# Kernel optimization log

Measured on AMD Instinct MI355X. Metric: run time of the kernel, lower is better.

Reference implementation:

```python
import jax, jax.numpy as jnp
import numpy as np

B, T, D, H, P, A = 128, 512, 512, 512, 512, 32  # envs, steps, feat, lstm hidden, latent, actions


def setup_inputs() -> dict:
    key = jax.random.key(0)
    ks = jax.random.split(key, 30)
    N = B * T
    lin = lambda k, o, i: 0.02 * jax.random.normal(k, (o, i), jnp.float32)
    vec = lambda k, o: 0.02 * jax.random.normal(k, (o,), jnp.float32)
    inp = {
        'features': jax.random.normal(ks[0], (N, D), jnp.float32),
        'episode_starts': (jax.random.uniform(ks[1], (N,)) < 0.02).astype(jnp.float32),
        'h0_pi': jax.random.normal(ks[2], (1, B, H), jnp.float32),
        'c0_pi': jax.random.normal(ks[3], (1, B, H), jnp.float32),
        'h0_vf': jax.random.normal(ks[4], (1, B, H), jnp.float32),
        'c0_vf': jax.random.normal(ks[5], (1, B, H), jnp.float32),
        'Wih_pi': lin(ks[6], 4 * H, D), 'Whh_pi': lin(ks[7], 4 * H, H),
        'bih_pi': vec(ks[8], 4 * H), 'bhh_pi': vec(ks[9], 4 * H),
        'Wih_vf': lin(ks[10], 4 * H, D), 'Whh_vf': lin(ks[11], 4 * H, H),
        'bih_vf': vec(ks[12], 4 * H), 'bhh_vf': vec(ks[13], 4 * H),
        'pol_w1': lin(ks[14], P, H), 'pol_b1': vec(ks[15], P),
        'pol_w2': lin(ks[16], P, P), 'pol_b2': vec(ks[17], P),
        'val_w1': lin(ks[18], P, H), 'val_b1': vec(ks[19], P),
        'val_w2': lin(ks[20], P, P), 'val_b2': vec(ks[21], P),
        'actor_w': lin(ks[22], A, P), 'actor_b': vec(ks[23], A),
        'critic_w': lin(ks[24], 1, P), 'critic_b': vec(ks[25], 1),
        'deterministic': 1,
    }
    return inp


def masked_lstm(xs, starts, h0, c0, Wih, Whh, bih, bhh):
    # xs: [T,B,D], starts: [T,B]; PyTorch gate order i,f,g,o; reset h,c where episode starts.
    def step(carry, inp):
        h, c = carry
        x, s = inp
        m = (1.0 - s)[:, None]
        h, c = h * m, c * m
        g = x @ Wih.T + bih + h @ Whh.T + bhh
        i, f, gg, o = jnp.split(g, 4, axis=-1)
        c = jax.nn.sigmoid(f) * c + jax.nn.sigmoid(i) * jnp.tanh(gg)
        h = jax.nn.sigmoid(o) * jnp.tanh(c)
        return (h, c), h
    (hT, cT), ys = jax.lax.scan(step, (h0[0], c0[0]), (xs, starts))
    return ys, hT[None], cT[None]


def mlp(x, w1, b1, w2, b2):
    return jax.nn.relu(x @ w1.T + b1) @ w2.T + b2


def reference(features, episode_starts, h0_pi, c0_pi, h0_vf, c0_vf,
              Wih_pi, Whh_pi, bih_pi, bhh_pi, Wih_vf, Whh_vf, bih_vf, bhh_vf,
              pol_w1, pol_b1, pol_w2, pol_b2, val_w1, val_b1, val_w2, val_b2,
              actor_w, actor_b, critic_w, critic_b, deterministic):
    n_seq = h0_pi.shape[1]
    d = features.shape[-1]
    xs = features.reshape(n_seq, -1, d).swapaxes(0, 1)        # [T,B,D]
    st = episode_starts.reshape(n_seq, -1).swapaxes(0, 1)     # [T,B]
    ys_pi, h_pi, c_pi = masked_lstm(xs, st, h0_pi, c0_pi, Wih_pi, Whh_pi, bih_pi, bhh_pi)
    ys_vf, h_vf, c_vf = masked_lstm(xs, st, h0_vf, c0_vf, Wih_vf, Whh_vf, bih_vf, bhh_vf)
    hsz = ys_pi.shape[-1]
    lat_pi = ys_pi.swapaxes(0, 1).reshape(-1, hsz)            # [B*T,H]
    lat_vf = ys_vf.swapaxes(0, 1).reshape(-1, hsz)
    lat_pi = mlp(lat_pi, pol_w1, pol_b1, pol_w2, pol_b2)
    lat_vf = mlp(lat_vf, val_w1, val_b1, val_w2, val_b2)
    values = lat_vf @ critic_w.T + critic_b                    # [B*T,1]
    logits = lat_pi @ actor_w.T + actor_b                      # [B*T,A]
    actions = jnp.argmax(logits, axis=-1)                      # deterministic mode
    logp = jax.nn.log_softmax(logits, axis=-1)
    log_prob = jnp.take_along_axis(logp, actions[:, None], axis=1)[:, 0]
    return actions, values, log_prob, h_pi, c_pi, h_vf, c_vf
```

## Files before the change

### kernel.cpp

```cpp
#include <hip/hip_runtime.h>
#include <math.h>

#define BB 128
#define TT 512
#define DD 512
#define HH 512
#define NN (BB*TT)
#define PP 512
#define AA 32
#define CH 64
#define CR (BB*CH)

typedef unsigned short u16;
typedef unsigned int   u32;
typedef __attribute__((ext_vector_type(8))) short short8;
typedef __attribute__((ext_vector_type(4))) float f32x4;

__device__ __forceinline__ u16 f2bf(float f){
    u32 x = __float_as_uint(f);
    u32 r = (x + 0x7fffu + ((x >> 16) & 1u)) >> 16;
    return (u16)r;
}
__device__ __forceinline__ float bf2f(u16 u){
    return __uint_as_float(((u32)u) << 16);
}
__device__ __forceinline__ f32x4 mfma16(short8 a, short8 b, f32x4 c){
    return __builtin_amdgcn_mfma_f32_16x16x32_bf16(a, b, c, 0, 0, 0);
}
__device__ __forceinline__ float sigm(float x){
    return 1.f/(1.f + __expf(-x));
}
__device__ __forceinline__ float tanh_f(float x){
    return 1.f - 2.f/(1.f + __expf(2.f*x));
}

__device__ __forceinline__ short8 ld_mall(const u16* p){
    short8 r;
    asm volatile("global_load_dwordx4 %0, %1, off sc0 sc1"
                 : "=&v"(r) : "v"(p) : "memory");
    return r;
}
__device__ __forceinline__ void st_mall(u16* p, short8 v){
    asm volatile("global_store_dwordx4 %0, %1, off sc0 sc1"
                 :: "v"(p), "v"(v) : "memory");
}

__device__ __forceinline__ unsigned a_add(unsigned* p){
    return __hip_atomic_fetch_add(p, 1u, __ATOMIC_RELAXED, __HIP_MEMORY_SCOPE_AGENT);
}
__device__ __forceinline__ unsigned a_ld(unsigned* p){
    return __hip_atomic_load(p, __ATOMIC_RELAXED, __HIP_MEMORY_SCOPE_AGENT);
}

#define BARZ_N 75264

__global__ __launch_bounds__(256) void prep_lstm_w(
    const float* __restrict__ Wih_pi, const float* __restrict__ Whh_pi,
    const float* __restrict__ bih_pi, const float* __restrict__ bhh_pi,
    const float* __restrict__ Wih_vf, const float* __restrict__ Whh_vf,
    const float* __restrict__ bih_vf, const float* __restrict__ bhh_vf,
    u16* __restrict__ wihHi, u16* __restrict__ wihLo,
    u16* __restrict__ whhHi, u16* __restrict__ whhLo,
    float* __restrict__ biasP)
{
    long i = (long)blockIdx.x*256 + threadIdx.x;
    if (i >= 2L*2048*512) return;
    int L = (int)(i >> 20);
    int rem = (int)(i & 1048575);
    int c = rem >> 9, k = rem & 511;
    int u = c >> 2, g = c & 3;
    long src = (long)(g*512 + u)*512 + k;
    float wih = (L ? Wih_vf : Wih_pi)[src];
    float whh = (L ? Whh_vf : Whh_pi)[src];
    u16 h1 = f2bf(wih); wihHi[i] = h1; wihLo[i] = f2bf(wih - bf2f(h1));
    u16 h2 = f2bf(whh); whhHi[i] = h2; whhLo[i] = f2bf(whh - bf2f(h2));
    if (k == 0) {
        float b = (L ? bih_vf : bih_pi)[g*512+u] + (L ? bhh_vf : bhh_pi)[g*512+u];
        biasP[L*2048 + c] = b;
    }
}

__global__ __launch_bounds__(256) void prep_mlp_w(
    const float* __restrict__ w1pi, const float* __restrict__ w1vf,
    const float* __restrict__ w2pi, const float* __restrict__ w2vf,
    const float* __restrict__ b1pi, const float* __restrict__ b1vf,
    const float* __restrict__ b2pi, const float* __restrict__ b2vf,
    u16* __restrict__ mHi, u16* __restrict__ mLo, float* __restrict__ biasM)
{
    long i = (long)blockIdx.x*256 + threadIdx.x;
    if (i >= 4L*262144) return;
    int mat = (int)(i >> 18);
    int rem = (int)(i & 262143);
    const float* src = mat==0 ? w1pi : mat==1 ? w1vf : mat==2 ? w2pi : w2vf;
    float v = src[rem];
    u16 h = f2bf(v); mHi[i] = h; mLo[i] = f2bf(v - bf2f(h));
    if (rem < 512) {
        const float* bs = mat==0 ? b1pi : mat==1 ? b1vf : mat==2 ? b2pi : b2vf;
        biasM[mat*512 + rem] = bs[rem];
    }
}

__global__ __launch_bounds__(256) void init_state_k(
    const float* __restrict__ h0_pi, const float* __restrict__ c0_pi,
    const float* __restrict__ h0_vf, const float* __restrict__ c0_vf,
    const float* __restrict__ starts,
    u16* __restrict__ hHi, u16* __restrict__ hLo, float* __restrict__ cT,
    float* __restrict__ startsT, unsigned* __restrict__ barZ)
{
    int i = blockIdx.x*256 + threadIdx.x;
    if (i < BARZ_N) barZ[i] = 0u;
    if (i < NN) {
        int e = i >> 9, t = i & 511;
        startsT[t*128 + e] = starts[i];
    }
    if (i >= 2*BB*HH) return;
    int L = i >> 16; int r = i & 65535;
    int e = r >> 9, u = r & 511;
    float m = 1.0f - starts[(long)e*TT];
    float h = (L ? h0_vf : h0_pi)[r] * m;
    float c = (L ? c0_vf : c0_pi)[r] * m;
    long hidx = (long)(L*2)*65536 + r;
    u16 hh = f2bf(h);
    hHi[hidx] = hh; hLo[hidx] = f2bf(h - bf2f(hh));
    cT[(long)L*65536 + (long)u*128 + e] = c;
}

template<int AM, int EM>
__global__ __launch_bounds__(256) void gemm_k512(
    const float* __restrict__ Afp,
    const u16* __restrict__ aHi, const u16* __restrict__ aLo, long aZ,
    int rowSh, int rowOuterHi, int rowOuterLo, int rowBase,
    const u16* __restrict__ bHi, const u16* __restrict__ bLo, long bZ,
    const float* __restrict__ bias, long biasZ,
    float* __restrict__ outF, long outFZ, int outLd,
    u16* __restrict__ oHi, u16* __restrict__ oLo, long oZ)
{
    __shared__ u16 sAh[5120], sAl[5120], sBh[5120], sBl[5120];
    const int tid = threadIdx.x;
    const int z = blockIdx.z;
    const long Mbase = (long)blockIdx.x * 128;
    const long Nbase = (long)blockIdx.y * 128;
    const int r2 = tid >> 1, half = tid & 1;
    const long mstage = Mbase + r2;
    const long arow = (mstage >> rowSh) * (long)rowOuterHi
                    + (mstage & (((long)1<<rowSh)-1)) * (long)rowOuterLo + rowBase;
    const long brow = Nbase + r2;
    const int wid = tid >> 6, lane = tid & 63;
    const int mh = wid & 1, nh = wid >> 1;
    const int l15 = lane & 15, quad = lane >> 4;

    f32x4 acc[4][4];
    #pragma unroll
    for (int i = 0; i < 4; ++i)
        #pragma unroll
        for (int j = 0; j < 4; ++j)
            acc[i][j] = (f32x4){0.f,0.f,0.f,0.f};

    const int sOffW = r2*40 + half*16;

    for (int kt = 0; kt < 16; ++kt) {
        const int k0 = kt*32;
        if constexpr (AM == 0) {
            const float* ap = Afp + arow*512 + k0 + half*16;
            float fv[16];
            #pragma unroll
            for (int q = 0; q < 4; ++q) *(float4*)(fv + q*4) = ((const float4*)ap)[q];
            short8 vh0, vh1, vl0, vl1;
            #pragma unroll
            for (int i = 0; i < 8; ++i){
                u16 h  = f2bf(fv[i]);   vh0[i] = (short)h;  vl0[i] = (short)f2bf(fv[i]   - bf2f(h));
                u16 h2 = f2bf(fv[8+i]); vh1[i] = (short)h2; vl1[i] = (short)f2bf(fv[8+i] - bf2f(h2));
            }
            *(short8*)(sAh + sOffW) = vh0; *(short8*)(sAh + sOffW + 8) = vh1;
            *(short8*)(sAl + sOffW) = vl0; *(short8*)(sAl + sOffW + 8) = vl1;
        } else {
            const u16* ph = aHi + (long)z*aZ + arow*512 + k0 + half*16;
            const u16* pl = aLo + (long)z*aZ + arow*512 + k0 + half*16;
            *(short8*)(sAh + sOffW) = *(const short8*)ph;
            *(short8*)(sAh + sOffW + 8) = *(const short8*)(ph + 8);
            *(short8*)(sAl + sOffW) = *(const short8*)pl;
            *(short8*)(sAl + sOffW + 8) = *(const short8*)(pl + 8);
        }
        {
            const u16* ph = bHi + (long)z*bZ + brow*512 + k0 + half*16;
            const u16* pl = bLo + (long)z*bZ + brow*512 + k0 + half*16;
            *(short8*)(sBh + sOffW) = *(const short8*)ph;
            *(short8*)(sBh + sOffW + 8) = *(const short8*)(ph + 8);
            *(short8*)(sBl + sOffW) = *(const short8*)pl;
            *(short8*)(sBl + sOffW + 8) = *(const short8*)(pl + 8);
        }
        __syncthreads();
        short8 bh[4], bl[4];
        #pragma unroll
        for (int nt = 0; nt < 4; ++nt){
            int bo = (nh*64 + nt*16 + l15)*40 + quad*8;
            bh[nt] = *(const short8*)(sBh + bo);
            bl[nt] = *(const short8*)(sBl + bo);
        }
        #pragma unroll
        for (int mt = 0; mt < 4; ++mt){
            int ao = (mh*64 + mt*16 + l15)*40 + quad*8;
            short8 ah = *(const short8*)(sAh + ao);
            short8 al = *(const short8*)(sAl + ao);
            #pragma unroll
            for (int nt = 0; nt < 4; ++nt){
                acc[mt][nt] = mfma16(ah, bh[nt], acc[mt][nt]);
                acc[mt][nt] = mfma16(ah, bl[nt], acc[mt][nt]);
                acc[mt][nt] = mfma16(al, bh[nt], acc[mt][nt]);
            }
        }
        __syncthreads();
    }
    #pragma unroll
    for (int nt = 0; nt < 4; ++nt){
        const long col = Nbase + nh*64 + nt*16 + l15;
        const float bv = bias[(long)z*biasZ + col];
        #pragma unroll
        for (int mt = 0; mt < 4; ++mt){
            const long rowm = Mbase + mh*64 + mt*16 + quad*4;
            #pragma unroll
            for (int rr = 0; rr < 4; ++rr){
                float v = acc[mt][nt][rr] + bv;
                const long m = rowm + rr;
                if constexpr (EM == 0) {
                    outF[(long)z*outFZ + m*(long)outLd + col] = v;
                } else {
                    if constexpr (EM == 1) v = fmaxf(v, 0.f);
                    u16 h = f2bf(v);
                    u16 l = f2bf(v - bf2f(h));
                    oHi[(long)z*oZ + m*512 + col] = h;
                    oLo[(long)z*oZ + m*512 + col] = l;
                }
            }
        }
    }
}

__global__ __launch_bounds__(256) void lstm_chunk(
    u16* __restrict__ hHi, u16* __restrict__ hLo,
    const u16* __restrict__ whhHi, const u16* __restrict__ whhLo,
    const float* __restrict__ gx,
    const float* __restrict__ startsT,
    float* __restrict__ cT,
    u16* __restrict__ ysHi, u16* __restrict__ ysLo,
    float* __restrict__ dout, unsigned* __restrict__ barZ, int t0)
{
    __shared__ __attribute__((aligned(16))) u16 sA[2][16384];
    __shared__ float zsm[4][144];
    __shared__ unsigned shLead, shNloc, shXC;

    const int tid  = threadIdx.x;
    const int wc   = blockIdx.x;
    const int eb   = blockIdx.y;
    const int L    = blockIdx.z;
    const int wid  = tid >> 6, lane = tid & 63;
    const int l15  = lane & 15, quad = lane >> 4;
    const int ebase = eb*64;
    const int e    = ebase + wid*16 + l15;

    unsigned xcc;
    asm("s_getreg_b32 %0, hwreg(HW_REG_XCC_ID)" : "=s"(xcc));
    xcc &= 7u;
    const int ch = t0 >> 6;
    unsigned* ARRb  = barZ;
    unsigned* DONEb = barZ + 65536;
    unsigned* RCNTb = barZ + 73728;
    unsigned* SBARb = barZ + 74752;
    unsigned* XCNTb = barZ + 74880;

    if (tid == 0){
        unsigned r = a_add(&RCNTb[(ch*8 + (int)xcc)*16]);
        shLead = (r == 0u) ? 1u : 0u;
        if (r == 0u){
            a_add(&XCNTb[ch*16]);
            asm volatile("s_waitcnt vmcnt(0)" ::: "memory");
        }
        a_add(&SBARb[ch*16]);
        while (a_ld(&SBARb[ch*16]) < 256u) __builtin_amdgcn_s_sleep(2);
        shNloc = a_ld(&RCNTb[(ch*8 + (int)xcc)*16]);
        shXC   = a_ld(&XCNTb[ch*16]);
    }

    {
        const size_t wbase = (size_t)L*1048576 + (size_t)(wc*32)*512;
        #pragma unroll
        for (int i = 0; i < 16; ++i){
            int f = tid + i*256;
            int pl = f >> 11;
            int r2 = f & 2047;
            int wcol = r2 >> 6, ksg = r2 & 63;
            const u16* src = (pl ? whhLo : whhHi) + wbase + (size_t)wcol*512 + ksg*8;
            int dst = (ksg>>2)*1024 + wcol*32 + (ksg&3)*8;
            *(short8*)(sA[pl] + dst) = *(const short8*)src;
        }
    }
    __syncthreads();
    const unsigned lead = shLead, nloc = shNloc, xcnt = shXC;

    const int u0 = wc*8 + quad;
    const int u1 = wc*8 + 4 + quad;
    const size_t ci0 = (size_t)L*65536 + (size_t)u0*128 + e;
    const size_t ci1 = (size_t)L*65536 + (size_t)u1*128 + e;
    float c0 = cT[ci0];
    float c1 = cT[ci1];

    const size_t hrowOff = (size_t)e*512 + quad*8;
    const size_t gxbase  = ((size_t)L*CR + e)*2048 + wc*32 + quad*4;

    float4 gv0 = *(const float4*)(gx + gxbase);
    float4 gv1 = *(const float4*)(gx + gxbase + 16);
    float mn = (t0 < TT-1) ? (1.0f - startsT[(t0+1)*128 + e]) : 1.0f;

    for (int tau = 0; tau < CH; ++tau){
        const int t = t0 + tau;
        const int p = t & 1;

        const u16* hHiP = hHi + (size_t)(L*2+p)*65536 + hrowOff;
        const u16* hLoP = hLo + (size_t)(L*2+p)*65536 + hrowOff;
        short8 pbh[16], pbl[16];
        #pragma unroll
        for (int i = 0; i < 16; ++i){
            pbh[i] = ld_mall(hHiP + i*32);
            pbl[i] = ld_mall(hLoP + i*32);
        }
        f32x4 acc0 = (f32x4){0.f,0.f,0.f,0.f};
        f32x4 acc1 = (f32x4){0.f,0.f,0.f,0.f};
        #pragma unroll
        for (int kt = 0; kt < 16; ++kt){
            if (kt == 0){
                asm volatile("s_waitcnt vmcnt(24)" ::: "memory");
                __builtin_amdgcn_sched_barrier(0);
            } else if (kt == 4){
                asm volatile("s_waitcnt vmcnt(16)" ::: "memory");
                __builtin_amdgcn_sched_barrier(0);
            } else if (kt == 8){
                asm volatile("s_waitcnt vmcnt(8)" ::: "memory");
                __builtin_amdgcn_sched_barrier(0);
            } else if (kt == 12){
                asm volatile("s_waitcnt vmcnt(0)" ::: "memory");
                __builtin_amdgcn_sched_barrier(0);
            }
            short8 bh = pbh[kt];
            short8 bl = pbl[kt];
            int a0 = kt*1024 + l15*32 + quad*8;
            short8 ah0 = *(const short8*)(sA[0] + a0);
            short8 al0 = *(const short8*)(sA[1] + a0);
            short8 ah1 = *(const short8*)(sA[0] + a0 + 512);
            short8 al1 = *(const short8*)(sA[1] + a0 + 512);
            acc0 = mfma16(ah0, bh, acc0);
            acc0 = mfma16(ah0, bl, acc0);
            acc0 = mfma16(al0, bh, acc0);
            acc1 = mfma16(ah1, bh, acc1);
            acc1 = mfma16(ah1, bl, acc1);
            acc1 = mfma16(al1, bh, acc1);
        }

        {
            float ii = sigm(acc0[0] + gv0.x);
            float ff = sigm(acc0[1] + gv0.y);
            float gg = tanh_f(acc0[2] + gv0.z);
            float oo = sigm(acc0[3] + gv0.w);
            float cn = ff*c0 + ii*gg;
            float hn = oo * tanh_f(cn);
            c0 = cn * mn;
            zsm[wid][l15*8 + quad] = hn;
            zsm[wid][128 + l15] = mn;
            if (t == TT-1) {
                dout[(size_t)(3+2*L)*NN + (size_t)e*512 + u0] = hn;
                dout[(size_t)(4+2*L)*NN + (size_t)e*512 + u0] = cn;
            }
        }
        {
            float ii = sigm(acc1[0] + gv1.x);
            float ff = sigm(acc1[1] + gv1.y);
            float gg = tanh_f(acc1[2] + gv1.z);
            float oo = sigm(acc1[3] + gv1.w);
            float cn = ff*c1 + ii*gg;
            float hn = oo * tanh_f(cn);
            c1 = cn * mn;
            zsm[wid][l15*8 + 4 + quad] = hn;
            if (t == TT-1) {
                dout[(size_t)(3+2*L)*NN + (size_t)e*512 + u1] = hn;
                dout[(size_t)(4+2*L)*NN + (size_t)e*512 + u1] = cn;
            }
        }
        __syncthreads();

        {
            const int g2 = quad;
            const int e2 = l15;
            const int eg = ebase + g2*16 + e2;
            float v[8];
            #pragma unroll
            for (int j = 0; j < 8; ++j) v[j] = zsm[g2][e2*8 + j];
            const float mn2 = zsm[g2][128 + e2];
            short8 pk;
            if (wid < 2) {
                #pragma unroll
                for (int j = 0; j < 8; ++j){
                    float hm = v[j] * mn2;
                    u16 h = f2bf(hm);
                    pk[j] = (short)(wid == 0 ? h : f2bf(hm - bf2f(h)));
                }
                u16* dst = (wid == 0 ? hHi : hLo)
                         + (size_t)(L*2 + (1-p))*65536 + (size_t)eg*512 + wc*8;
                st_mall(dst, pk);
                asm volatile("s_waitcnt vmcnt(0)" ::: "memory");
            } else {
                #pragma unroll
                for (int j = 0; j < 8; ++j){
                    u16 h = f2bf(v[j]);
                    pk[j] = (short)(wid == 2 ? h : f2bf(v[j] - bf2f(h)));
                }
                u16* dst = (wid == 2 ? ysHi : ysLo)
                         + ((size_t)L*CR + (size_t)tau*128 + eg)*512 + wc*8;
                *(short8*)dst = pk;
            }
        }

        __builtin_amdgcn_s_barrier();
        if (tau < CH-1){
            if (tid == 0) a_add(&ARRb[((size_t)t*8 + xcc)*16]);
            const float* gpn = gx + gxbase + (size_t)(tau+1)*(128*2048);
            gv0 = *(const float4*)(gpn);
            gv1 = *(const float4*)(gpn + 16);
            mn = (t+1 < TT-1) ? (1.0f - startsT[(t+2)*128 + e]) : 1.0f;
            if (tid == 0){
                unsigned* ap = &ARRb[((size_t)t*8 + xcc)*16];
                unsigned* dp = &DONEb[(size_t)t*16];
                if (lead){
                    while (a_ld(ap) < nloc) __builtin_amdgcn_s_sleep(1);
                    a_add(dp);
                }
                while (a_ld(dp) < xcnt) __builtin_amdgcn_s_sleep(1);
            }
            __builtin_amdgcn_s_barrier();
            asm volatile("" ::: "memory");
        }
    }

    cT[ci0] = c0;
    cT[ci1] = c1;
}

__global__ __launch_bounds__(256) void head_pi(
    const u16* __restrict__ latHi, const u16* __restrict__ latLo,
    const float* __restrict__ actor_w, const float* __restrict__ actor_b,
    float* __restrict__ dout, int t0)
{
    __shared__ float latS[16*516];
    __shared__ float lg[16*36];
    const int tid = threadIdx.x;
    const long r0 = (long)blockIdx.x * 16;
    {
        int rr = tid >> 4, seg = tid & 15;
        const u16* ph = latHi + (r0 + rr)*512 + seg*32;
        const u16* pl = latLo + (r0 + rr)*512 + seg*32;
        float* dst = latS + rr*516 + seg*32;
        #pragma unroll
        for (int ii = 0; ii < 4; ++ii){
            short8 vh = *(const short8*)(ph + ii*8);
            short8 vl = *(const short8*)(pl + ii*8);
            #pragma unroll
            for (int jj = 0; jj < 8; ++jj)
                dst[ii*8+jj] = bf2f((u16)vh[jj]) + bf2f((u16)vl[jj]);
        }
    }
    __syncthreads();
    {
        int rr = tid >> 4, a0 = (tid & 15)*2;
        const float4* lrow = (const float4*)(latS + rr*516);
        float acc0 = actor_b[a0], acc1 = actor_b[a0+1];
        for (int kq = 0; kq < 128; ++kq){
            float4 lv = lrow[kq];
            float4 w0 = ((const float4*)actor_w)[(a0  )*128 + kq];
            float4 w1 = ((const float4*)actor_w)[(a0+1)*128 + kq];
            acc0 += lv.x*w0.x + lv.y*w0.y + lv.z*w0.z + lv.w*w0.w;
            acc1 += lv.x*w1.x + lv.y*w1.y + lv.z*w1.z + lv.w*w1.w;
        }
        lg[rr*36 + a0]   = acc0;
        lg[rr*36 + a0+1] = acc1;
    }
    __syncthreads();
    if (tid < 16){
        float mx = -INFINITY; int am = 0;
        #pragma unroll
        for (int a = 0; a < AA; ++a){
            float v = lg[tid*36 + a];
            if (v > mx){ mx = v; am = a; }
        }
        float se = 0.f;
        #pragma unroll
        for (int a = 0; a < AA; ++a) se += expf(lg[tid*36 + a] - mx);
        long row = r0 + tid;
        long n = (row & 127)*TT + t0 + (row >> 7);
        dout[n] = (float)am;
        dout[2L*NN + n] = -logf(se);
    }
}

__global__ __launch_bounds__(256) void head_vf(
    const u16* __restrict__ latHi, const u16* __restrict__ latLo,
    const float* __restrict__ critic_w, const float* __restrict__ critic_b,
    float* __restrict__ dout, int t0)
{
    __shared__ float part[256];
    const int tid = threadIdx.x;
    const long r0 = (long)blockIdx.x * 32;
    int rr = tid >> 3, seg = tid & 7;
    const u16* ph = latHi + (r0 + rr)*512 + seg*64;
    const u16* pl = latLo + (r0 + rr)*512 + seg*64;
    float acc = 0.f;
    #pragma unroll
    for (int ii = 0; ii < 8; ++ii){
        short8 vh = *(const short8*)(ph + ii*8);
        short8 vl = *(const short8*)(pl + ii*8);
        #pragma unroll
        for (int jj = 0; jj < 8; ++jj){
            float lv = bf2f((u16)vh[jj]) + bf2f((u16)vl[jj]);
            acc += lv * critic_w[seg*64 + ii*8 + jj];
        }
    }
    part[tid] = acc;
    __syncthreads();
    if (tid < 32){
        float v = critic_b[0];
        #pragma unroll
        for (int s = 0; s < 8; ++s) v += part[tid*8 + s];
        long row = r0 + tid;
        long n = (row & 127)*TT + t0 + (row >> 7);
        dout[(long)NN + n] = v;
    }
}

extern "C" void kernel_launch(void* const* d_in, const int* in_sizes, int n_in,
                              void* d_out, int out_size, void* d_ws, size_t ws_size,
                              hipStream_t stream) {
    const float* features = (const float*)d_in[0];
    const float* starts   = (const float*)d_in[1];
    const float* h0_pi = (const float*)d_in[2];
    const float* c0_pi = (const float*)d_in[3];
    const float* h0_vf = (const float*)d_in[4];
    const float* c0_vf = (const float*)d_in[5];
    const float* Wih_pi = (const float*)d_in[6];
    const float* Whh_pi = (const float*)d_in[7];
    const float* bih_pi = (const float*)d_in[8];
    const float* bhh_pi = (const float*)d_in[9];
    const float* Wih_vf = (const float*)d_in[10];
    const float* Whh_vf = (const float*)d_in[11];
    const float* bih_vf = (const float*)d_in[12];
    const float* bhh_vf = (const float*)d_in[13];
    const float* pol_w1 = (const float*)d_in[14];
    const float* pol_b1 = (const float*)d_in[15];
    const float* pol_w2 = (const float*)d_in[16];
    const float* pol_b2 = (const float*)d_in[17];
    const float* val_w1 = (const float*)d_in[18];
    const float* val_b1 = (const float*)d_in[19];
    const float* val_w2 = (const float*)d_in[20];
    const float* val_b2 = (const float*)d_in[21];
    const float* actor_w  = (const float*)d_in[22];
    const float* actor_b  = (const float*)d_in[23];
    const float* critic_w = (const float*)d_in[24];
    const float* critic_b = (const float*)d_in[25];
    float* out = (float*)d_out;

    size_t off = 0;
    auto alloc = [&](size_t b) {
        void* p = (char*)d_ws + off;
        off += (b + 255) & ~(size_t)255;
        return p;
    };
    u16* wihHi = (u16*)alloc(2L*2048*512*2);
    u16* wihLo = (u16*)alloc(2L*2048*512*2);
    u16* whhHi = (u16*)alloc(2L*2048*512*2);
    u16* whhLo = (u16*)alloc(2L*2048*512*2);
    float* biasP = (float*)alloc(2L*2048*4);
    u16* mHi = (u16*)alloc(4L*262144*2);
    u16* mLo = (u16*)alloc(4L*262144*2);
    float* biasM = (float*)alloc(4L*512*4);
    u16* hHi = (u16*)alloc(2L*2*128*512*2);
    u16* hLo = (u16*)alloc(2L*2*128*512*2);
    float* cT  = (float*)alloc(2L*128*512*4);
    float* startsT = (float*)alloc((size_t)NN*4);
    unsigned* barZ = (unsigned*)alloc((size_t)BARZ_N*4);
    u16* ysHi = (u16*)alloc(2L*CR*512*2);
    u16* ysLo = (u16*)alloc(2L*CR*512*2);
    u16* hidHi = (u16*)alloc(2L*CR*512*2);
    u16* hidLo = (u16*)alloc(2L*CR*512*2);
    u16* latHi = (u16*)alloc(2L*CR*512*2);
    u16* latLo = (u16*)alloc(2L*CR*512*2);
    float* gxF = (float*)alloc(2L*CR*2048*4);
    const long gxZ = (long)CR*2048;
    const long pZ  = (long)CR*512;

    prep_lstm_w<<<dim3(8192), dim3(256), 0, stream>>>(
        Wih_pi, Whh_pi, bih_pi, bhh_pi, Wih_vf, Whh_vf, bih_vf, bhh_vf,
        wihHi, wihLo, whhHi, whhLo, biasP);
    prep_mlp_w<<<dim3(4096), dim3(256), 0, stream>>>(
        pol_w1, val_w1, pol_w2, val_w2, pol_b1, val_b1, pol_b2, val_b2,
        mHi, mLo, biasM);
    init_state_k<<<dim3(512), dim3(256), 0, stream>>>(
        h0_pi, c0_pi, h0_vf, c0_vf, starts, hHi, hLo, cT, startsT, barZ);

    for (int t0 = 0; t0 < TT; t0 += CH) {
        gemm_k512<0,0><<<dim3(CR/128, 16, 2), dim3(256), 0, stream>>>(
            features, nullptr, nullptr, 0L,
            7, 1, 512, t0,
            wihHi, wihLo, 1048576L,
            biasP, 2048L,
            gxF, gxZ, 2048,
            nullptr, nullptr, 0L);
        lstm_chunk<<<dim3(64, 2, 2), dim3(256), 0, stream>>>(
            hHi, hLo, whhHi, whhLo, gxF, startsT, cT, ysHi, ysLo,
            out, barZ, t0);
        gemm_k512<1,1><<<dim3(CR/128, 4, 2), dim3(256), 0, stream>>>(
            nullptr, ysHi, ysLo, pZ,
            30, 0, 1, 0,
            mHi, mLo, 262144L,
            biasM, 512L,
            nullptr, 0L, 0,
            hidHi, hidLo, pZ);
        gemm_k512<1,2><<<dim3(CR/128, 4, 2), dim3(256), 0, stream>>>(
            nullptr, hidHi, hidLo, pZ,
            30, 0, 1, 0,
            mHi + 2L*262144, mLo + 2L*262144, 262144L,
            biasM + 1024, 512L,
            nullptr, 0L, 0,
            latHi, latLo, pZ);
        head_pi<<<dim3(CR/16), dim3(256), 0, stream>>>(
            latHi, latLo, actor_w, actor_b, out, t0);
        head_vf<<<dim3(CR/32), dim3(256), 0, stream>>>(
            latHi + pZ, latLo + pZ, critic_w, critic_b, out, t0);
    }
}
```

Baseline: 6.713 ms.

## Re-tile LSTM recurrent step with split-K waves and reduction through shared memory

The persistent LSTM block now owns 64 gate columns and 32 envs instead of 32 columns and 64 envs. Each wave handles half of K for all four column tiles, and the partial sums are combined through shared memory. Only the hi part of Whh stays in LDS, while the lo part is read from global/L2 each step. This halves the per-wave h loads from global and changes the grid to 32x4x2. The cost is an extra __syncthreads and reduction each step, plus global reads of Whh-lo on the critical path.

```diff
diff --git a/kernel.cpp b/kernel.cpp
--- a/kernel.cpp
+++ b/kernel.cpp
@@ -245,18 +245,21 @@
     u16* __restrict__ ysHi, u16* __restrict__ ysLo,
     float* __restrict__ dout, unsigned* __restrict__ barZ, int t0)
 {
-    __shared__ __attribute__((aligned(16))) u16 sA[2][16384];
-    __shared__ float zsm[4][144];
+    __shared__ __attribute__((aligned(16))) u16 sA[32768];
+    __shared__ __attribute__((aligned(16))) float red[2][64][20];
+    __shared__ float zsm[32][17];
+    __shared__ float mns[32];
     __shared__ unsigned shLead, shNloc, shXC;
 
     const int tid  = threadIdx.x;
-    const int wc   = blockIdx.x;
-    const int eb   = blockIdx.y;
+    const int wcb  = blockIdx.x;
+    const int eq   = blockIdx.y;
     const int L    = blockIdx.z;
     const int wid  = tid >> 6, lane = tid & 63;
     const int l15  = lane & 15, quad = lane >> 4;
-    const int ebase = eb*64;
-    const int e    = ebase + wid*16 + l15;
+    const int ee   = wid & 1;
+    const int kh   = wid >> 1;
+    const int e    = eq*32 + ee*16 + l15;
 
     unsigned xcc;
     asm("s_getreg_b32 %0, hwreg(HW_REG_XCC_ID)" : "=s"(xcc));
@@ -281,34 +284,35 @@
         shXC   = a_ld(&XCNTb[ch*16]);
     }
 
+    const size_t wbase = (size_t)L*1048576 + (size_t)(wcb*64)*512;
     {
-        const size_t wbase = (size_t)L*1048576 + (size_t)(wc*32)*512;
         #pragma unroll
         for (int i = 0; i < 16; ++i){
             int f = tid + i*256;
-            int pl = f >> 11;
-            int r2 = f & 2047;
-            int wcol = r2 >> 6, ksg = r2 & 63;
-            const u16* src = (pl ? whhLo : whhHi) + wbase + (size_t)wcol*512 + ksg*8;
-            int dst = (ksg>>2)*1024 + wcol*32 + (ksg&3)*8;
-            *(short8*)(sA[pl] + dst) = *(const short8*)src;
+            int col = f >> 6, kc = f & 63;
+            const u16* src = whhHi + wbase + (size_t)col*512 + kc*8;
+            int dst = (kc>>2)*2048 + col*32 + (kc&3)*8;
+            *(short8*)(sA + dst) = *(const short8*)src;
         }
     }
     __syncthreads();
     const unsigned lead = shLead, nloc = shNloc, xcnt = shXC;
 
-    const int u0 = wc*8 + quad;
-    const int u1 = wc*8 + 4 + quad;
-    const size_t ci0 = (size_t)L*65536 + (size_t)u0*128 + e;
-    const size_t ci1 = (size_t)L*65536 + (size_t)u1*128 + e;
-    float c0 = cT[ci0];
-    float c1 = cT[ci1];
+    const int ct0 = kh*2;
+    int   u_[2]; size_t ci_[2]; float creg[2];
+    #pragma unroll
+    for (int j = 0; j < 2; ++j){
+        u_[j]  = wcb*16 + (ct0+j)*4 + quad;
+        ci_[j] = (size_t)L*65536 + (size_t)u_[j]*128 + e;
+        creg[j] = cT[ci_[j]];
+    }
 
     const size_t hrowOff = (size_t)e*512 + quad*8;
-    const size_t gxbase  = ((size_t)L*CR + e)*2048 + wc*32 + quad*4;
-
-    float4 gv0 = *(const float4*)(gx + gxbase);
-    float4 gv1 = *(const float4*)(gx + gxbase + 16);
+    const size_t gxrow0  = ((size_t)L*CR + e)*2048 + wcb*64 + quad*4;
+    const u16*   loBase  = whhLo + wbase + quad*8;
+
+    float4 gvA = *(const float4*)(gx + gxrow0 + (ct0  )*16);
+    float4 gvB = *(const float4*)(gx + gxrow0 + (ct0+1)*16);
     float mn = (t0 < TT-1) ? (1.0f - startsT[(t0+1)*128 + e]) : 1.0f;
 
     for (int tau = 0; tau < CH; ++tau){
@@ -317,83 +321,70 @@
 
         const u16* hHiP = hHi + (size_t)(L*2+p)*65536 + hrowOff;
         const u16* hLoP = hLo + (size_t)(L*2+p)*65536 + hrowOff;
-        short8 pbh[16], pbl[16];
-        #pragma unroll
-        for (int i = 0; i < 16; ++i){
-            pbh[i] = ld_mall(hHiP + i*32);
-            pbl[i] = ld_mall(hLoP + i*32);
-        }
-        f32x4 acc0 = (f32x4){0.f,0.f,0.f,0.f};
-        f32x4 acc1 = (f32x4){0.f,0.f,0.f,0.f};
-        #pragma unroll
-        for (int kt = 0; kt < 16; ++kt){
-            if (kt == 0){
-                asm volatile("s_waitcnt vmcnt(24)" ::: "memory");
-                __builtin_amdgcn_sched_barrier(0);
-            } else if (kt == 4){
-                asm volatile("s_waitcnt vmcnt(16)" ::: "memory");
-                __builtin_amdgcn_sched_barrier(0);
-            } else if (kt == 8){
-                asm volatile("s_waitcnt vmcnt(8)" ::: "memory");
-                __builtin_amdgcn_sched_barrier(0);
-            } else if (kt == 12){
-                asm volatile("s_waitcnt vmcnt(0)" ::: "memory");
-                __builtin_amdgcn_sched_barrier(0);
+        short8 pbh[8], pbl[8];
+        #pragma unroll
+        for (int i = 0; i < 8; ++i){
+            const int koff = (kh*8 + i)*32;
+            pbh[i] = ld_mall(hHiP + koff);
+            pbl[i] = ld_mall(hLoP + koff);
+        }
+        asm volatile("s_waitcnt vmcnt(0)" ::: "memory");
+        __builtin_amdgcn_sched_barrier(0);
+
+        f32x4 acc[4];
+        #pragma unroll
+        for (int ct = 0; ct < 4; ++ct) acc[ct] = (f32x4){0.f,0.f,0.f,0.f};
+        #pragma unroll
+        for (int i = 0; i < 8; ++i){
+            const int ktg = kh*8 + i;
+            short8 bh = pbh[i];
+            short8 bl = pbl[i];
+            #pragma unroll
+            for (int ct = 0; ct < 4; ++ct){
+                short8 ah = *(const short8*)(sA + ktg*2048 + (ct*16 + l15)*32 + quad*8);
+                short8 al = *(const short8*)(loBase + (size_t)(ct*16 + l15)*512 + ktg*32);
+                acc[ct] = mfma16(ah, bh, acc[ct]);
+                acc[ct] = mfma16(ah, bl, acc[ct]);
+                acc[ct] = mfma16(al, bh, acc[ct]);
             }
-            short8 bh = pbh[kt];
-            short8 bl = pbl[kt];
-            int a0 = kt*1024 + l15*32 + quad*8;
-            short8 ah0 = *(const short8*)(sA[0] + a0);
-            short8 al0 = *(const short8*)(sA[1] + a0);
-            short8 ah1 = *(const short8*)(sA[0] + a0 + 512);
-            short8 al1 = *(const short8*)(sA[1] + a0 + 512);
-            acc0 = mfma16(ah0, bh, acc0);
-            acc0 = mfma16(ah0, bl, acc0);
-            acc0 = mfma16(al0, bh, acc0);
-            acc1 = mfma16(ah1, bh, acc1);
-            acc1 = mfma16(ah1, bl, acc1);
-            acc1 = mfma16(al1, bh, acc1);
         }
 
         {
-            float ii = sigm(acc0[0] + gv0.x);
-            float ff = sigm(acc0[1] + gv0.y);
-            float gg = tanh_f(acc0[2] + gv0.z);
-            float oo = sigm(acc0[3] + gv0.w);
-            float cn = ff*c0 + ii*gg;
+            const int cw = (1-kh)*2;
+            *(f32x4*)&red[ee][lane][(cw  )*4] = acc[cw];
+            *(f32x4*)&red[ee][lane][(cw+1)*4] = acc[cw+1];
+        }
+        __syncthreads();
+
+        #pragma unroll
+        for (int j = 0; j < 2; ++j){
+            const int ct = ct0 + j;
+            f32x4 z = acc[ct] + *(const f32x4*)&red[ee][lane][ct*4];
+            float4 gv = j ? gvB : gvA;
+            float ii = sigm(z[0] + gv.x);
+            float ff = sigm(z[1] + gv.y);
+            float gg = tanh_f(z[2] + gv.z);
+            float oo = sigm(z[3] + gv.w);
+            float cn = ff*creg[j] + ii*gg;
             float hn = oo * tanh_f(cn);
-            c0 = cn * mn;
-            zsm[wid][l15*8 + quad] = hn;
-            zsm[wid][128 + l15] = mn;
+            creg[j] = cn * mn;
+            zsm[ee*16 + l15][ct*4 + quad] = hn;
             if (t == TT-1) {
-                dout[(size_t)(3+2*L)*NN + (size_t)e*512 + u0] = hn;
-                dout[(size_t)(4+2*L)*NN + (size_t)e*512 + u0] = cn;
+                dout[(size_t)(3+2*L)*NN + (size_t)e*512 + u_[j]] = hn;
+                dout[(size_t)(4+2*L)*NN + (size_t)e*512 + u_[j]] = cn;
             }
         }
+        if (kh == 0 && quad == 0) mns[ee*16 + l15] = mn;
+        __syncthreads();
+
         {
-            float ii = sigm(acc1[0] + gv1.x);
-            float ff = sigm(acc1[1] + gv1.y);
-            float gg = tanh_f(acc1[2] + gv1.z);
-            float oo = sigm(acc1[3] + gv1.w);
-            float cn = ff*c1 + ii*gg;
-            float hn = oo * tanh_f(cn);
-            c1 = cn * mn;
-            zsm[wid][l15*8 + 4 + quad] = hn;
-            if (t == TT-1) {
-                dout[(size_t)(3+2*L)*NN + (size_t)e*512 + u1] = hn;
-                dout[(size_t)(4+2*L)*NN + (size_t)e*512 + u1] = cn;
-            }
-        }
-        __syncthreads();
-
-        {
-            const int g2 = quad;
-            const int e2 = l15;
-            const int eg = ebase + g2*16 + e2;
+            const int el = lane >> 1;
+            const int uh = (lane & 1)*8;
+            const int eg = eq*32 + el;
             float v[8];
             #pragma unroll
-            for (int j = 0; j < 8; ++j) v[j] = zsm[g2][e2*8 + j];
-            const float mn2 = zsm[g2][128 + e2];
+            for (int j = 0; j < 8; ++j) v[j] = zsm[el][uh + j];
+            const float mn2 = mns[el];
             short8 pk;
             if (wid < 2) {
                 #pragma unroll
@@ -403,7 +394,7 @@
                     pk[j] = (short)(wid == 0 ? h : f2bf(hm - bf2f(h)));
                 }
                 u16* dst = (wid == 0 ? hHi : hLo)
-                         + (size_t)(L*2 + (1-p))*65536 + (size_t)eg*512 + wc*8;
+                         + (size_t)(L*2 + (1-p))*65536 + (size_t)eg*512 + wcb*16 + uh;
                 st_mall(dst, pk);
                 asm volatile("s_waitcnt vmcnt(0)" ::: "memory");
             } else {
@@ -413,7 +404,7 @@
                     pk[j] = (short)(wid == 2 ? h : f2bf(v[j] - bf2f(h)));
                 }
                 u16* dst = (wid == 2 ? ysHi : ysLo)
-                         + ((size_t)L*CR + (size_t)tau*128 + eg)*512 + wc*8;
+                         + ((size_t)L*CR + (size_t)tau*128 + eg)*512 + wcb*16 + uh;
                 *(short8*)dst = pk;
             }
         }
@@ -421,9 +412,9 @@
         __builtin_amdgcn_s_barrier();
         if (tau < CH-1){
             if (tid == 0) a_add(&ARRb[((size_t)t*8 + xcc)*16]);
-            const float* gpn = gx + gxbase + (size_t)(tau+1)*(128*2048);
-            gv0 = *(const float4*)(gpn);
-            gv1 = *(const float4*)(gpn + 16);
+            const size_t gxn = gxrow0 + (size_t)(tau+1)*(128*2048);
+            gvA = *(const float4*)(gx + gxn + (ct0  )*16);
+            gvB = *(const float4*)(gx + gxn + (ct0+1)*16);
             mn = (t+1 < TT-1) ? (1.0f - startsT[(t+2)*128 + e]) : 1.0f;
             if (tid == 0){
                 unsigned* ap = &ARRb[((size_t)t*8 + xcc)*16];
@@ -439,8 +430,8 @@
         }
     }
 
-    cT[ci0] = c0;
-    cT[ci1] = c1;
+    cT[ci_[0]] = creg[0];
+    cT[ci_[1]] = creg[1];
 }
 
 __global__ __launch_bounds__(256) void head_pi(
@@ -610,7 +601,7 @@
             biasP, 2048L,
             gxF, gxZ, 2048,
             nullptr, nullptr, 0L);
-        lstm_chunk<<<dim3(64, 2, 2), dim3(256), 0, stream>>>(
+        lstm_chunk<<<dim3(32, 4, 2), dim3(256), 0, stream>>>(
             hHi, hLo, whhHi, whhLo, gxF, startsT, cT, ysHi, ysLo,
             out, barZ, t0);
         gemm_k512<1,1><<<dim3(CR/128, 4, 2), dim3(256), 0, stream>>>(
```

Result: slower. 8.226 ms (+22.5%).
